# Kernel tuning notes

Measured on AMD Instinct MI355X. Metric: run time of the kernel, lower is better.

## Reference

```python
import jax, jax.numpy as jnp
import numpy as np

E = 8        # num_local_experts
H = 1024     # hidden_dim
F = 4096     # intermediate_dim
T = 16384    # total permuted tokens (sum of tokens_per_expert)


def setup_inputs() -> dict:
    key = jax.random.key(0)
    k_x, k_w1, k_w2 = jax.random.split(key, 3)
    x = jax.random.normal(k_x, (T, H), dtype=jnp.float32)
    # Ragged tokens-per-expert summing exactly to T (variable group sizes).
    rng = np.random.default_rng(0)
    bounds = np.sort(rng.integers(0, T, size=E - 1))
    counts = np.diff(np.concatenate([[0], bounds, [T]])).astype(np.int32)
    tokens_per_expert = jnp.asarray(counts)  # [E], int32, sums to T
    # xavier_normal_ init per expert matrix: std = sqrt(2/(fan_in+fan_out))
    std = (2.0 / (H + F)) ** 0.5
    weight1 = jax.random.normal(k_w1, (E, H, F), dtype=jnp.float32) * std  # fc1
    weight2 = jax.random.normal(k_w2, (E, F, H), dtype=jnp.float32) * std  # fc2
    return {
        "permuted_local_hidden_states": x,
        "weight1": weight1,
        "weight2": weight2,
        "tokens_per_expert": tokens_per_expert,
    }


def reference(permuted_local_hidden_states, weight1, weight2, tokens_per_expert):
    # Grouped GEMM: rows of x are grouped contiguously by expert; group e uses
    # weight[e]. lax.ragged_dot is the exact analogue of gg.ops.gmm(trans_b=False).
    fc1 = jax.lax.ragged_dot(permuted_local_hidden_states, weight1,
                             tokens_per_expert)            # [T, F]
    act = jax.nn.gelu(fc1, approximate=False)               # activation fused between GEMMs
    fc2 = jax.lax.ragged_dot(act, weight2, tokens_per_expert)  # [T, H]
    return fc2
```

## Files before the change

### kernel.cpp

```cpp
#include <hip/hip_runtime.h>
#include <hip/hip_bf16.h>

#define E_NUM 8
#define H_DIM 1024
#define F_DIM 4096
#define T_TOK 16384

#define NT 256
#define MT_MAX (T_TOK / 128 + E_NUM)
#define MT256 (T_TOK / 256 + E_NUM)

typedef __attribute__((ext_vector_type(8))) short bf16x8;
typedef __attribute__((ext_vector_type(4))) float f32x4;

__device__ __forceinline__ short f2bf(float f) {
    unsigned u = __builtin_bit_cast(unsigned, f);
    u += 0x7FFFu + ((u >> 16) & 1u);
    return (short)(u >> 16);
}

__device__ __forceinline__ float exp2_fast(float a) {
#if __has_builtin(__builtin_amdgcn_exp2f)
    return __builtin_amdgcn_exp2f(a);
#else
    return exp2f(a);
#endif
}
__device__ __forceinline__ float rcp_fast(float a) {
#if __has_builtin(__builtin_amdgcn_rcpf)
    return __builtin_amdgcn_rcpf(a);
#else
    return 1.0f / a;
#endif
}

__device__ __forceinline__ float fast_gelu(float x) {
    float x2 = x * x;
    float y = x * (0.7978845608f + 0.0356774081f * x2);
    float z = exp2_fast(y * 2.8853900817779268f);
    float r = rcp_fast(z + 1.0f);
    return x * (1.0f - r);
}

__device__ __forceinline__ void gload16(const void* g, void* l) {
    __builtin_amdgcn_global_load_lds(
        (const __attribute__((address_space(1))) void*)g,
        (__attribute__((address_space(3))) void*)l, 16, 0, 0);
}

template<int N>
__device__ __forceinline__ void vmwait() {
    if constexpr (N == 0) asm volatile("s_waitcnt vmcnt(0)" ::: "memory");
    else if constexpr (N == 4) asm volatile("s_waitcnt vmcnt(4)" ::: "memory");
    else if constexpr (N == 8) asm volatile("s_waitcnt vmcnt(8)" ::: "memory");
}

__device__ __forceinline__ void lgkm0() {
    asm volatile("s_waitcnt lgkmcnt(0)" ::: "memory");
}

__device__ __forceinline__ void bar() {
    asm volatile("s_barrier" ::: "memory");
}

__device__ __forceinline__ void tile_map128(const int* __restrict__ cnt, int mt,
                                            int& row0, int& rend, int& e_out) {
    int acc = 0, off = 0;
    e_out = -1;
    for (int i = 0; i < E_NUM; ++i) {
        int c = cnt[i];
        int nti = (c + 127) >> 7;
        if (mt < acc + nti) {
            e_out = i; row0 = off + (mt - acc) * 128; rend = off + c; return;
        }
        acc += nti; off += c;
    }
}

__device__ __forceinline__ void tile_map256(const int* __restrict__ cnt, int mt,
                                            int& row0, int& rend, int& e_out) {
    int acc = 0, off = 0;
    e_out = -1;
    for (int i = 0; i < E_NUM; ++i) {
        int c = cnt[i];
        int nti = (c + 255) >> 8;
        if (mt < acc + nti) {
            e_out = i; row0 = off + (mt - acc) * 256; rend = off + c; return;
        }
        acc += nti; off += c;
    }
}

__global__ __launch_bounds__(NT)
void cvt_x_kernel(const float* __restrict__ in, short* __restrict__ out, int n8) {
    int i = blockIdx.x * blockDim.x + threadIdx.x;
    const int stride = gridDim.x * blockDim.x;
    for (; i < n8; i += stride) {
        f32x4 f0 = ((const f32x4*)in)[(size_t)i * 2];
        f32x4 f1 = ((const f32x4*)in)[(size_t)i * 2 + 1];
        bf16x8 v;
        v[0] = f2bf(f0[0]); v[1] = f2bf(f0[1]); v[2] = f2bf(f0[2]); v[3] = f2bf(f0[3]);
        v[4] = f2bf(f1[0]); v[5] = f2bf(f1[1]); v[6] = f2bf(f1[2]); v[7] = f2bf(f1[3]);
        ((bf16x8*)out)[i] = v;
    }
}

__global__ __launch_bounds__(NT)
void transpose_cvt(const float* __restrict__ in, short* __restrict__ out,
                   int R, int C) {
    __shared__ short tb[64][72];
    const int e = blockIdx.z;
    const float* ine = in + (size_t)e * R * C;
    short* oute = out + (size_t)e * R * C;
    const int c0 = blockIdx.x * 64, r0 = blockIdx.y * 64;
    const int t = threadIdx.x;
    const int rl = t >> 4, cl = (t & 15) * 4;
#pragma unroll
    for (int p = 0; p < 4; ++p) {
        int r = rl + p * 16;
        f32x4 f = *(const f32x4*)(ine + (size_t)(r0 + r) * C + c0 + cl);
#pragma unroll
        for (int j = 0; j < 4; ++j) tb[cl + j][r] = f2bf(f[j]);
    }
    __syncthreads();
    const int c2 = t >> 3, rc = (t & 7) * 8;
#pragma unroll
    for (int p = 0; p < 2; ++p) {
        int c = c2 + p * 32;
        bf16x8 v = *(const bf16x8*)&tb[c][rc];
        *(bf16x8*)(oute + (size_t)(c0 + c) * R + r0 + rc) = v;
    }
}

#define RING_RD_A(mh, SA)                                                     \
    _Pragma("unroll") for (int f = 0; f < 4; ++f) {                           \
        const int r_ = ((mh) * 4 + f) * 32 + wm * 16 + lr;                    \
        const int u_ = r_ * 4 + (lg ^ ((r_ >> 1) & 3));                       \
        areg[f] = ((const bf16x8*)(SA))[u_];                                  \
    }

#define RING_RD_B(SB)                                                         \
    _Pragma("unroll") for (int g = 0; g < 4; ++g) {                           \
        const int r_ = g * 64 + wn * 16 + lr;                                 \
        const int u_ = r_ * 4 + (lg ^ ((r_ >> 1) & 3));                       \
        breg[g] = ((const bf16x8*)(SB))[u_];                                  \
    }

#define RING_MM(mh)                                                           \
    _Pragma("unroll") for (int f = 0; f < 4; ++f)                             \
    _Pragma("unroll") for (int g = 0; g < 4; ++g)                             \
        acc[(mh) * 4 + f][g] = __builtin_amdgcn_mfma_f32_16x16x32_bf16(       \
            areg[f], breg[g], acc[(mh) * 4 + f][g], 0, 0, 0);

#define RING_STAGE_A(slot)                                                    \
    { short* base_ = lds + (slot) * SLOT;                                     \
      gload16(ag[0], base_ + d0); ag[0] += 32;                                \
      gload16(ag[1], base_ + d1); ag[1] += 32; }

#define RING_STAGE_B(slot)                                                    \
    { short* base_ = lds + (slot) * SLOT + 8192;                              \
      gload16(bg[0], base_ + d0); bg[0] += 32;                                \
      gload16(bg[1], base_ + d1); bg[1] += 32; }

template<bool GELU, int LDC, int NTX, int LDK>
__global__ __launch_bounds__(512, 2)
void gemm_ring(const short* __restrict__ A, const short* __restrict__ Bw,
               const int* __restrict__ cnt, void* __restrict__ Cout) {
    constexpr int SLOT = 16384;
    constexpr int KT = LDK / 32;
    static_assert(KT >= 4, "need at least 4 K-tiles");

    __shared__ __align__(16) short lds[2 * SLOT];

    constexpr int TOT = NTX * MT256;
    static_assert(TOT % 8 == 0, "grid must be divisible by 8 XCDs");
    constexpr int CPX = TOT / 8;
    const int lin = blockIdx.x;
    const int wg = (lin & 7) * CPX + (lin >> 3);
    const int mt = wg / NTX;
    const int nt = wg - mt * NTX;

    int row0, rend, e;
    tile_map256(cnt, mt, row0, rend, e);
    if (e < 0) return;
    const int n0 = nt * 256;
    const short* Be = Bw + (size_t)e * ((size_t)F_DIM * H_DIM);

    const int tid = threadIdx.x;
    const int lane = tid & 63;
    const int lr = lane & 15;
    const int lg = lane >> 4;
    const int w = tid >> 6;
    const int wm = w >> 2;
    const int wn = w & 3;

    const short* ag[2];
    const short* bg[2];
#pragma unroll
    for (int p = 0; p < 2; ++p) {
        int s = p * 512 + tid;
        int r = s >> 2;
        int kc = (s & 3) ^ ((r >> 1) & 3);
        int grow = row0 + r;
        if (grow >= T_TOK) grow = T_TOK - 1;
        ag[p] = A + (size_t)grow * LDK + kc * 8;
        bg[p] = Be + (size_t)(n0 + r) * LDK + kc * 8;
    }
    const int d0 = (0 * 512 + tid) * 8;
    const int d1 = (1 * 512 + tid) * 8;

    f32x4 acc[8][4];
#pragma unroll
    for (int i = 0; i < 8; ++i)
#pragma unroll
        for (int j = 0; j < 4; ++j) acc[i][j] = (f32x4){0.f, 0.f, 0.f, 0.f};
    bf16x8 areg[4];
    bf16x8 breg[4];

    RING_STAGE_A(0) RING_STAGE_B(0)
    RING_STAGE_A(1) RING_STAGE_B(1)
    vmwait<4>();
    bar();

    int kt = 0;
    for (; kt < KT - 2; ++kt) {
        const short* Sa = lds + (kt & 1) * SLOT;
        const short* Sb = Sa + 8192;
        RING_RD_B(Sb)
        RING_RD_A(0, Sa)
        __builtin_amdgcn_s_setprio(1);
        RING_MM(0)
        __builtin_amdgcn_s_setprio(0);
        RING_RD_A(1, Sa)
        __builtin_amdgcn_s_setprio(1);
        RING_MM(1)
        __builtin_amdgcn_s_setprio(0);
        lgkm0();
        bar();
        RING_STAGE_A(kt & 1)
        RING_STAGE_B(kt & 1)
        vmwait<4>();
        bar();
    }

    {
        const short* Sa = lds + (kt & 1) * SLOT;
        const short* Sb = Sa + 8192;
        RING_RD_B(Sb) RING_RD_A(0, Sa) RING_MM(0)
        RING_RD_A(1, Sa) RING_MM(1)
        vmwait<0>();
        bar();
        ++kt;
    }
    {
        const short* Sa = lds + (kt & 1) * SLOT;
        const short* Sb = Sa + 8192;
        RING_RD_B(Sb) RING_RD_A(0, Sa) RING_MM(0)
        RING_RD_A(1, Sa) RING_MM(1)
    }

#pragma unroll
    for (int f = 0; f < 8; ++f) {
#pragma unroll
        for (int g = 0; g < 4; ++g) {
            const int gcol = n0 + g * 64 + wn * 16 + lr;
#pragma unroll
            for (int rr = 0; rr < 4; ++rr) {
                const int grow = row0 + f * 32 + wm * 16 + lg * 4 + rr;
                if (grow < rend) {
                    float v = acc[f][g][rr];
                    if constexpr (GELU) {
                        ((short*)Cout)[(size_t)grow * LDC + gcol] = f2bf(fast_gelu(v));
                    } else {
                        ((float*)Cout)[(size_t)grow * LDC + gcol] = v;
                    }
                }
            }
        }
    }
}

__global__ __launch_bounds__(NT)
void gemm1_kernel(const float* __restrict__ X, const float* __restrict__ W1,
                  const int* __restrict__ cnt, short* __restrict__ act) {
    __shared__ short Alds[128 * 64];
    __shared__ short Blds[128 * 64];

    int row0, rend, e;
    tile_map128(cnt, blockIdx.y, row0, rend, e);
    if (e < 0) return;

    const int n0 = blockIdx.x * 128;
    const float* W = W1 + (size_t)e * H_DIM * F_DIM;

    const int tid = threadIdx.x;
    const int lane = tid & 63;
    const int w = tid >> 6;
    const int wr = (w >> 1) * 64;
    const int wc = (w & 1) * 64;
    const int lr = lane & 15;
    const int lg = lane >> 4;

    const int a_r0 = tid >> 3;
    const int a_kc = tid & 7;
    const int b_n = tid & 127;
    const int b_kg = (tid >> 7) * 8;

    f32x4 acc[4][4];
#pragma unroll
    for (int i = 0; i < 4; ++i)
#pragma unroll
        for (int j = 0; j < 4; ++j) acc[i][j] = (f32x4){0.f, 0.f, 0.f, 0.f};

    for (int kt = 0; kt < H_DIM / 64; ++kt) {
        const int k0 = kt * 64;
#pragma unroll
        for (int p = 0; p < 4; ++p) {
            int r = a_r0 + 32 * p;
            int grow = row0 + r;
            if (grow > T_TOK - 1) grow = T_TOK - 1;
            const float* src = X + (size_t)grow * H_DIM + k0 + a_kc * 8;
            f32x4 f0 = *(const f32x4*)src;
            f32x4 f1 = *(const f32x4*)(src + 4);
            bf16x8 v;
            v[0] = f2bf(f0[0]); v[1] = f2bf(f0[1]); v[2] = f2bf(f0[2]); v[3] = f2bf(f0[3]);
            v[4] = f2bf(f1[0]); v[5] = f2bf(f1[1]); v[6] = f2bf(f1[2]); v[7] = f2bf(f1[3]);
            ((bf16x8*)Alds)[(r * 8 + a_kc) ^ (r & 7)] = v;
        }
#pragma unroll
        for (int p = 0; p < 4; ++p) {
            int kb = p * 16 + b_kg;
            const float* src = W + (size_t)(k0 + kb) * F_DIM + n0 + b_n;
            bf16x8 v;
#pragma unroll
            for (int j = 0; j < 8; ++j) v[j] = f2bf(src[(size_t)j * F_DIM]);
            ((bf16x8*)Blds)[(b_n * 8 + (kb >> 3)) ^ (b_n & 7)] = v;
        }
        __syncthreads();
#pragma unroll
        for (int kk = 0; kk < 2; ++kk) {
            bf16x8 af[4], bfr[4];
#pragma unroll
            for (int fm = 0; fm < 4; ++fm) {
                int r = wr + fm * 16 + lr;
                af[fm] = ((bf16x8*)Alds)[(r * 8 + kk * 4 + lg) ^ (r & 7)];
            }
#pragma unroll
            for (int fn = 0; fn < 4; ++fn) {
                int n = wc + fn * 16 + lr;
                bfr[fn] = ((bf16x8*)Blds)[(n * 8 + kk * 4 + lg) ^ (n & 7)];
            }
#pragma unroll
            for (int fm = 0; fm < 4; ++fm)
#pragma unroll
                for (int fn = 0; fn < 4; ++fn)
                    acc[fm][fn] = __builtin_amdgcn_mfma_f32_16x16x32_bf16(
                        af[fm], bfr[fn], acc[fm][fn], 0, 0, 0);
        }
        __syncthreads();
    }

#pragma unroll
    for (int fm = 0; fm < 4; ++fm)
#pragma unroll
        for (int fn = 0; fn < 4; ++fn) {
            int gcol = n0 + wc + fn * 16 + lr;
#pragma unroll
            for (int rr = 0; rr < 4; ++rr) {
                int grow = row0 + wr + fm * 16 + lg * 4 + rr;
                if (grow < rend)
                    act[(size_t)grow * F_DIM + gcol] = f2bf(fast_gelu(acc[fm][fn][rr]));
            }
        }
}

__global__ __launch_bounds__(NT)
void gemm2_kernel(const short* __restrict__ ACT, const float* __restrict__ W2,
                  const int* __restrict__ cnt, float* __restrict__ out) {
    __shared__ short Alds[128 * 64];
    __shared__ short Blds[128 * 64];

    int row0, rend, e;
    tile_map128(cnt, blockIdx.y, row0, rend, e);
    if (e < 0) return;

    const int n0 = blockIdx.x * 128;
    const float* W = W2 + (size_t)e * F_DIM * H_DIM;

    const int tid = threadIdx.x;
    const int lane = tid & 63;
    const int w = tid >> 6;
    const int wr = (w >> 1) * 64;
    const int wc = (w & 1) * 64;
    const int lr = lane & 15;
    const int lg = lane >> 4;

    const int a_r0 = tid >> 3;
    const int a_kc = tid & 7;
    const int b_n = tid & 127;
    const int b_kg = (tid >> 7) * 8;

    f32x4 acc[4][4];
#pragma unroll
    for (int i = 0; i < 4; ++i)
#pragma unroll
        for (int j = 0; j < 4; ++j) acc[i][j] = (f32x4){0.f, 0.f, 0.f, 0.f};

    for (int kt = 0; kt < F_DIM / 64; ++kt) {
        const int k0 = kt * 64;
#pragma unroll
        for (int p = 0; p < 4; ++p) {
            int r = a_r0 + 32 * p;
            int grow = row0 + r;
            if (grow > T_TOK - 1) grow = T_TOK - 1;
            bf16x8 v = *(const bf16x8*)(ACT + (size_t)grow * F_DIM + k0 + a_kc * 8);
            ((bf16x8*)Alds)[(r * 8 + a_kc) ^ (r & 7)] = v;
        }
#pragma unroll
        for (int p = 0; p < 4; ++p) {
            int kb = p * 16 + b_kg;
            const float* src = W + (size_t)(k0 + kb) * H_DIM + n0 + b_n;
            bf16x8 v;
#pragma unroll
            for (int j = 0; j < 8; ++j) v[j] = f2bf(src[(size_t)j * H_DIM]);
            ((bf16x8*)Blds)[(b_n * 8 + (kb >> 3)) ^ (b_n & 7)] = v;
        }
        __syncthreads();
#pragma unroll
        for (int kk = 0; kk < 2; ++kk) {
            bf16x8 af[4], bfr[4];
#pragma unroll
            for (int fm = 0; fm < 4; ++fm) {
                int r = wr + fm * 16 + lr;
                af[fm] = ((bf16x8*)Alds)[(r * 8 + kk * 4 + lg) ^ (r & 7)];
            }
#pragma unroll
            for (int fn = 0; fn < 4; ++fn) {
                int n = wc + fn * 16 + lr;
                bfr[fn] = ((bf16x8*)Blds)[(n * 8 + kk * 4 + lg) ^ (n & 7)];
            }
#pragma unroll
            for (int fm = 0; fm < 4; ++fm)
#pragma unroll
                for (int fn = 0; fn < 4; ++fn)
                    acc[fm][fn] = __builtin_amdgcn_mfma_f32_16x16x32_bf16(
                        af[fm], bfr[fn], acc[fm][fn], 0, 0, 0);
        }
        __syncthreads();
    }

#pragma unroll
    for (int fm = 0; fm < 4; ++fm)
#pragma unroll
        for (int fn = 0; fn < 4; ++fn) {
            int gcol = n0 + wc + fn * 16 + lr;
#pragma unroll
            for (int rr = 0; rr < 4; ++rr) {
                int grow = row0 + wr + fm * 16 + lg * 4 + rr;
                if (grow < rend) out[(size_t)grow * H_DIM + gcol] = acc[fm][fn][rr];
            }
        }
}

extern "C" void kernel_launch(void* const* d_in, const int* in_sizes, int n_in,
                              void* d_out, int out_size, void* d_ws, size_t ws_size,
                              hipStream_t stream) {
    const float* x  = (const float*)d_in[0];
    const float* w1 = (const float*)d_in[1];
    const float* w2 = (const float*)d_in[2];
    const int* cnt  = (const int*)d_in[3];
    float* out = (float*)d_out;

    const size_t ACT_B = (size_t)T_TOK * F_DIM * 2;
    const size_t WT_B  = (size_t)E_NUM * F_DIM * H_DIM * 2;
    const size_t XB_B  = (size_t)T_TOK * H_DIM * 2;

    if (ws_size >= ACT_B + WT_B + XB_B) {
        short* act = (short*)d_ws;
        short* wt  = (short*)((char*)d_ws + ACT_B);
        short* xb  = (short*)((char*)d_ws + ACT_B + WT_B);

        cvt_x_kernel<<<2048, NT, 0, stream>>>(x, xb, T_TOK * H_DIM / 8);
        transpose_cvt<<<dim3(F_DIM / 64, H_DIM / 64, E_NUM), NT, 0, stream>>>(
            w1, wt, H_DIM, F_DIM);
        gemm_ring<true, F_DIM, 16, H_DIM>
            <<<16 * MT256, 512, 0, stream>>>(xb, wt, cnt, (void*)act);
        transpose_cvt<<<dim3(H_DIM / 64, F_DIM / 64, E_NUM), NT, 0, stream>>>(
            w2, wt, F_DIM, H_DIM);
        gemm_ring<false, H_DIM, 4, F_DIM>
            <<<4 * MT256, 512, 0, stream>>>(act, wt, cnt, (void*)out);
    } else if (ws_size >= ACT_B) {
        short* act = (short*)d_ws;
        gemm1_kernel<<<dim3(F_DIM / 128, MT_MAX), NT, 0, stream>>>(x, w1, cnt, act);
        gemm2_kernel<<<dim3(H_DIM / 128, MT_MAX), NT, 0, stream>>>(act, w2, cnt, out);
    }
}
```

Baseline: 529.4 us.

## Replace 256x256 double-buffered GEMM with 128x128 triple-buffered ring kernel

Swaps the 512-thread 256x256-tile GEMM with two LDS buffers for a 256-thread 128x128-tile kernel that keeps three LDS slots. Global-to-LDS loads for the next-but-one K tile are issued in the middle of the MFMA sequence, which removes one barrier per iteration. Smaller tiles also waste fewer padded rows at ragged expert boundaries and allow three blocks per CU. The cost is lower data reuse per tile, so more global and LDS traffic per FLOP.

```diff
diff --git a/kernel.cpp b/kernel.cpp
--- a/kernel.cpp
+++ b/kernel.cpp
@@ -8,7 +8,6 @@
 
 #define NT 256
 #define MT_MAX (T_TOK / 128 + E_NUM)
-#define MT256 (T_TOK / 256 + E_NUM)
 
 typedef __attribute__((ext_vector_type(8))) short bf16x8;
 typedef __attribute__((ext_vector_type(4))) float f32x4;
@@ -53,10 +52,6 @@
     if constexpr (N == 0) asm volatile("s_waitcnt vmcnt(0)" ::: "memory");
     else if constexpr (N == 4) asm volatile("s_waitcnt vmcnt(4)" ::: "memory");
     else if constexpr (N == 8) asm volatile("s_waitcnt vmcnt(8)" ::: "memory");
-}
-
-__device__ __forceinline__ void lgkm0() {
-    asm volatile("s_waitcnt lgkmcnt(0)" ::: "memory");
 }
 
 __device__ __forceinline__ void bar() {
@@ -72,20 +67,6 @@
         int nti = (c + 127) >> 7;
         if (mt < acc + nti) {
             e_out = i; row0 = off + (mt - acc) * 128; rend = off + c; return;
-        }
-        acc += nti; off += c;
-    }
-}
-
-__device__ __forceinline__ void tile_map256(const int* __restrict__ cnt, int mt,
-                                            int& row0, int& rend, int& e_out) {
-    int acc = 0, off = 0;
-    e_out = -1;
-    for (int i = 0; i < E_NUM; ++i) {
-        int c = cnt[i];
-        int nti = (c + 255) >> 8;
-        if (mt < acc + nti) {
-            e_out = i; row0 = off + (mt - acc) * 256; rend = off + c; return;
         }
         acc += nti; off += c;
     }
@@ -132,47 +113,47 @@
     }
 }
 
-#define RING_RD_A(mh, SA)                                                     \
-    _Pragma("unroll") for (int f = 0; f < 4; ++f) {                           \
-        const int r_ = ((mh) * 4 + f) * 32 + wm * 16 + lr;                    \
+#define R3_RD_A(SA)                                                           \
+    _Pragma("unroll") for (int fm = 0; fm < 4; ++fm) {                        \
+        const int r_ = wr + fm * 16 + lr;                                     \
         const int u_ = r_ * 4 + (lg ^ ((r_ >> 1) & 3));                       \
-        areg[f] = ((const bf16x8*)(SA))[u_];                                  \
-    }
-
-#define RING_RD_B(SB)                                                         \
-    _Pragma("unroll") for (int g = 0; g < 4; ++g) {                           \
-        const int r_ = g * 64 + wn * 16 + lr;                                 \
-        const int u_ = r_ * 4 + (lg ^ ((r_ >> 1) & 3));                       \
-        breg[g] = ((const bf16x8*)(SB))[u_];                                  \
-    }
-
-#define RING_MM(mh)                                                           \
-    _Pragma("unroll") for (int f = 0; f < 4; ++f)                             \
-    _Pragma("unroll") for (int g = 0; g < 4; ++g)                             \
-        acc[(mh) * 4 + f][g] = __builtin_amdgcn_mfma_f32_16x16x32_bf16(       \
-            areg[f], breg[g], acc[(mh) * 4 + f][g], 0, 0, 0);
-
-#define RING_STAGE_A(slot)                                                    \
-    { short* base_ = lds + (slot) * SLOT;                                     \
-      gload16(ag[0], base_ + d0); ag[0] += 32;                                \
-      gload16(ag[1], base_ + d1); ag[1] += 32; }
-
-#define RING_STAGE_B(slot)                                                    \
-    { short* base_ = lds + (slot) * SLOT + 8192;                              \
-      gload16(bg[0], base_ + d0); bg[0] += 32;                                \
-      gload16(bg[1], base_ + d1); bg[1] += 32; }
+        af[fm] = ((const bf16x8*)(SA))[u_];                                   \
+    }
+
+#define R3_RD_B(SB)                                                           \
+    _Pragma("unroll") for (int fn = 0; fn < 4; ++fn) {                        \
+        const int n_ = wc + fn * 16 + lr;                                     \
+        const int u_ = n_ * 4 + (lg ^ ((n_ >> 1) & 3));                       \
+        bf[fn] = ((const bf16x8*)(SB))[u_];                                   \
+    }
+
+#define R3_MM_H(h)                                                            \
+    _Pragma("unroll") for (int fm = 0; fm < 4; ++fm)                          \
+    _Pragma("unroll") for (int fn = (h) * 2; fn < (h) * 2 + 2; ++fn)          \
+        acc[fm][fn] = __builtin_amdgcn_mfma_f32_16x16x32_bf16(                \
+            af[fm], bf[fn], acc[fm][fn], 0, 0, 0);
+
+#define R3_ST_A(slot)                                                         \
+    { short* b_ = lds + (slot) * SLOT;                                        \
+      gload16(ag[0], b_ + tid * 8);         ag[0] += 32;                      \
+      gload16(ag[1], b_ + (256 + tid) * 8); ag[1] += 32; }
+
+#define R3_ST_B(slot)                                                         \
+    { short* b_ = lds + (slot) * SLOT + 4096;                                 \
+      gload16(bg[0], b_ + tid * 8);         bg[0] += 32;                      \
+      gload16(bg[1], b_ + (256 + tid) * 8); bg[1] += 32; }
 
 template<bool GELU, int LDC, int NTX, int LDK>
-__global__ __launch_bounds__(512, 2)
-void gemm_ring(const short* __restrict__ A, const short* __restrict__ Bw,
-               const int* __restrict__ cnt, void* __restrict__ Cout) {
-    constexpr int SLOT = 16384;
+__global__ __launch_bounds__(256, 3)
+void gemm_r3(const short* __restrict__ A, const short* __restrict__ Bw,
+             const int* __restrict__ cnt, void* __restrict__ Cout) {
+    constexpr int SLOT = 8192;
     constexpr int KT = LDK / 32;
-    static_assert(KT >= 4, "need at least 4 K-tiles");
-
-    __shared__ __align__(16) short lds[2 * SLOT];
-
-    constexpr int TOT = NTX * MT256;
+    static_assert(KT >= 3, "need at least 3 K-tiles");
+
+    __shared__ __align__(16) short lds[3 * SLOT];
+
+    constexpr int TOT = NTX * MT_MAX;
     static_assert(TOT % 8 == 0, "grid must be divisible by 8 XCDs");
     constexpr int CPX = TOT / 8;
     const int lin = blockIdx.x;
@@ -181,9 +162,9 @@
     const int nt = wg - mt * NTX;
 
     int row0, rend, e;
-    tile_map256(cnt, mt, row0, rend, e);
+    tile_map128(cnt, mt, row0, rend, e);
     if (e < 0) return;
-    const int n0 = nt * 256;
+    const int n0 = nt * 128;
     const short* Be = Bw + (size_t)e * ((size_t)F_DIM * H_DIM);
 
     const int tid = threadIdx.x;
@@ -191,14 +172,14 @@
     const int lr = lane & 15;
     const int lg = lane >> 4;
     const int w = tid >> 6;
-    const int wm = w >> 2;
-    const int wn = w & 3;
+    const int wr = (w >> 1) * 64;
+    const int wc = (w & 1) * 64;
 
     const short* ag[2];
     const short* bg[2];
 #pragma unroll
     for (int p = 0; p < 2; ++p) {
-        int s = p * 512 + tid;
+        int s = p * 256 + tid;
         int r = s >> 2;
         int kc = (s & 3) ^ ((r >> 1) & 3);
         int grow = row0 + r;
@@ -206,69 +187,67 @@
         ag[p] = A + (size_t)grow * LDK + kc * 8;
         bg[p] = Be + (size_t)(n0 + r) * LDK + kc * 8;
     }
-    const int d0 = (0 * 512 + tid) * 8;
-    const int d1 = (1 * 512 + tid) * 8;
-
-    f32x4 acc[8][4];
-#pragma unroll
-    for (int i = 0; i < 8; ++i)
+
+    f32x4 acc[4][4];
+#pragma unroll
+    for (int i = 0; i < 4; ++i)
 #pragma unroll
         for (int j = 0; j < 4; ++j) acc[i][j] = (f32x4){0.f, 0.f, 0.f, 0.f};
-    bf16x8 areg[4];
-    bf16x8 breg[4];
-
-    RING_STAGE_A(0) RING_STAGE_B(0)
-    RING_STAGE_A(1) RING_STAGE_B(1)
+    bf16x8 af[4];
+    bf16x8 bf[4];
+
+    R3_ST_A(0) R3_ST_B(0)
+    R3_ST_A(1) R3_ST_B(1)
     vmwait<4>();
     bar();
 
-    int kt = 0;
-    for (; kt < KT - 2; ++kt) {
-        const short* Sa = lds + (kt & 1) * SLOT;
-        const short* Sb = Sa + 8192;
-        RING_RD_B(Sb)
-        RING_RD_A(0, Sa)
+    int s_rd = 0;
+    int s_st = 2;
+    for (int kt = 0; kt < KT - 2; ++kt) {
+        const short* Sa = lds + s_rd * SLOT;
+        const short* Sb = Sa + 4096;
+        R3_RD_B(Sb)
+        R3_RD_A(Sa)
+        R3_ST_A(s_st)
         __builtin_amdgcn_s_setprio(1);
-        RING_MM(0)
+        R3_MM_H(0)
         __builtin_amdgcn_s_setprio(0);
-        RING_RD_A(1, Sa)
+        R3_ST_B(s_st)
         __builtin_amdgcn_s_setprio(1);
-        RING_MM(1)
+        R3_MM_H(1)
         __builtin_amdgcn_s_setprio(0);
-        lgkm0();
-        bar();
-        RING_STAGE_A(kt & 1)
-        RING_STAGE_B(kt & 1)
+        s_rd = (s_rd == 2) ? 0 : s_rd + 1;
+        s_st = (s_st == 2) ? 0 : s_st + 1;
         vmwait<4>();
         bar();
     }
 
     {
-        const short* Sa = lds + (kt & 1) * SLOT;
-        const short* Sb = Sa + 8192;
-        RING_RD_B(Sb) RING_RD_A(0, Sa) RING_MM(0)
-        RING_RD_A(1, Sa) RING_MM(1)
+        const short* Sa = lds + s_rd * SLOT;
+        const short* Sb = Sa + 4096;
+        R3_RD_B(Sb) R3_RD_A(Sa)
+        R3_MM_H(0) R3_MM_H(1)
+        s_rd = (s_rd == 2) ? 0 : s_rd + 1;
         vmwait<0>();
         bar();
-        ++kt;
     }
     {
-        const short* Sa = lds + (kt & 1) * SLOT;
-        const short* Sb = Sa + 8192;
-        RING_RD_B(Sb) RING_RD_A(0, Sa) RING_MM(0)
-        RING_RD_A(1, Sa) RING_MM(1)
-    }
-
-#pragma unroll
-    for (int f = 0; f < 8; ++f) {
-#pragma unroll
-        for (int g = 0; g < 4; ++g) {
-            const int gcol = n0 + g * 64 + wn * 16 + lr;
+        const short* Sa = lds + s_rd * SLOT;
+        const short* Sb = Sa + 4096;
+        R3_RD_B(Sb) R3_RD_A(Sa)
+        R3_MM_H(0) R3_MM_H(1)
+    }
+
+#pragma unroll
+    for (int fm = 0; fm < 4; ++fm) {
+#pragma unroll
+        for (int fn = 0; fn < 4; ++fn) {
+            const int gcol = n0 + wc + fn * 16 + lr;
 #pragma unroll
             for (int rr = 0; rr < 4; ++rr) {
-                const int grow = row0 + f * 32 + wm * 16 + lg * 4 + rr;
+                const int grow = row0 + wr + fm * 16 + lg * 4 + rr;
                 if (grow < rend) {
-                    float v = acc[f][g][rr];
+                    float v = acc[fm][fn][rr];
                     if constexpr (GELU) {
                         ((short*)Cout)[(size_t)grow * LDC + gcol] = f2bf(fast_gelu(v));
                     } else {
@@ -339,23 +318,23 @@
         __syncthreads();
 #pragma unroll
         for (int kk = 0; kk < 2; ++kk) {
-            bf16x8 af[4], bfr[4];
+            bf16x8 af2[4], bf2[4];
 #pragma unroll
             for (int fm = 0; fm < 4; ++fm) {
                 int r = wr + fm * 16 + lr;
-                af[fm] = ((bf16x8*)Alds)[(r * 8 + kk * 4 + lg) ^ (r & 7)];
+                af2[fm] = ((bf16x8*)Alds)[(r * 8 + kk * 4 + lg) ^ (r & 7)];
             }
 #pragma unroll
             for (int fn = 0; fn < 4; ++fn) {
                 int n = wc + fn * 16 + lr;
-                bfr[fn] = ((bf16x8*)Blds)[(n * 8 + kk * 4 + lg) ^ (n & 7)];
+                bf2[fn] = ((bf16x8*)Blds)[(n * 8 + kk * 4 + lg) ^ (n & 7)];
             }
 #pragma unroll
             for (int fm = 0; fm < 4; ++fm)
 #pragma unroll
                 for (int fn = 0; fn < 4; ++fn)
                     acc[fm][fn] = __builtin_amdgcn_mfma_f32_16x16x32_bf16(
-                        af[fm], bfr[fn], acc[fm][fn], 0, 0, 0);
+                        af2[fm], bf2[fn], acc[fm][fn], 0, 0, 0);
         }
         __syncthreads();
     }
@@ -428,23 +407,23 @@
         __syncthreads();
 #pragma unroll
         for (int kk = 0; kk < 2; ++kk) {
-            bf16x8 af[4], bfr[4];
+            bf16x8 af2[4], bf2[4];
 #pragma unroll
             for (int fm = 0; fm < 4; ++fm) {
                 int r = wr + fm * 16 + lr;
-                af[fm] = ((bf16x8*)Alds)[(r * 8 + kk * 4 + lg) ^ (r & 7)];
+                af2[fm] = ((bf16x8*)Alds)[(r * 8 + kk * 4 + lg) ^ (r & 7)];
             }
 #pragma unroll
             for (int fn = 0; fn < 4; ++fn) {
                 int n = wc + fn * 16 + lr;
-                bfr[fn] = ((bf16x8*)Blds)[(n * 8 + kk * 4 + lg) ^ (n & 7)];
+                bf2[fn] = ((bf16x8*)Blds)[(n * 8 + kk * 4 + lg) ^ (n & 7)];
             }
 #pragma unroll
             for (int fm = 0; fm < 4; ++fm)
 #pragma unroll
                 for (int fn = 0; fn < 4; ++fn)
                     acc[fm][fn] = __builtin_amdgcn_mfma_f32_16x16x32_bf16(
-                        af[fm], bfr[fn], acc[fm][fn], 0, 0, 0);
+                        af2[fm], bf2[fn], acc[fm][fn], 0, 0, 0);
         }
         __syncthreads();
     }
@@ -483,12 +462,12 @@
         cvt_x_kernel<<<2048, NT, 0, stream>>>(x, xb, T_TOK * H_DIM / 8);
         transpose_cvt<<<dim3(F_DIM / 64, H_DIM / 64, E_NUM), NT, 0, stream>>>(
             w1, wt, H_DIM, F_DIM);
-        gemm_ring<true, F_DIM, 16, H_DIM>
-            <<<16 * MT256, 512, 0, stream>>>(xb, wt, cnt, (void*)act);
+        gemm_r3<true, F_DIM, 32, H_DIM>
+            <<<32 * MT_MAX, 256, 0, stream>>>(xb, wt, cnt, (void*)act);
         transpose_cvt<<<dim3(H_DIM / 64, F_DIM / 64, E_NUM), NT, 0, stream>>>(
             w2, wt, F_DIM, H_DIM);
-        gemm_ring<false, H_DIM, 4, F_DIM>
-            <<<4 * MT256, 512, 0, stream>>>(act, wt, cnt, (void*)out);
+        gemm_r3<false, H_DIM, 8, F_DIM>
+            <<<8 * MT_MAX, 256, 0, stream>>>(act, wt, cnt, (void*)out);
     } else if (ws_size >= ACT_B) {
         short* act = (short*)d_ws;
         gemm1_kernel<<<dim3(F_DIM / 128, MT_MAX), NT, 0, stream>>>(x, w1, cnt, act);
```

New measurement: 496.5 us. 6.2% less time.
